# Performance work log

Measured on AMD Instinct MI355X. Metric: run time of the kernel, lower is better.

Reference implementation:

```python
import jax, jax.numpy as jnp
import numpy as np

BETA = 0.25
K = 1024   # num_codebook_vectors
D = 256    # latent_dim


def setup_inputs() -> dict:
    key = jax.random.key(0)
    k1, k2 = jax.random.split(key)
    z = jax.random.normal(k1, (16, D, 64, 64), dtype=jnp.float32)
    # embedding initialized uniform(-1/K, 1/K) as in the torch module
    emb = jax.random.uniform(k2, (K, D), dtype=jnp.float32, minval=-1.0 / K, maxval=1.0 / K)
    return {"z": z, "emb": emb}


def reference(z, emb):
    sg = jax.lax.stop_gradient
    # NCHW -> NHWC
    z_nhwc = jnp.transpose(z, (0, 2, 3, 1))            # [B,H,W,D]
    zf = z_nhwc.reshape(-1, D)                          # [N,D]
    # squared euclidean distances: ||z||^2 + ||e||^2 - 2 z e^T
    d = (jnp.sum(zf * zf, axis=1, keepdims=True)
         + jnp.sum(emb * emb, axis=1)
         - 2.0 * jnp.matmul(zf, emb.T))                 # [N,K]
    min_encoding_indices = jnp.argmin(d, axis=1)        # [N] int
    z_q = emb[min_encoding_indices].reshape(z_nhwc.shape)  # [B,H,W,D]
    # loss exactly as in source (first term is zero in value, faithful)
    loss = (jnp.mean((sg(z_nhwc) - z_nhwc) ** 2)
            + BETA * jnp.mean((z_q - sg(z_nhwc)) ** 2))
    # straight-through estimator
    z_q_st = z_nhwc + sg(z_q - z_nhwc)
    out = jnp.transpose(z_q_st, (0, 3, 1, 2))           # NHWC -> NCHW
    return out, min_encoding_indices, loss
```

## Files before the change

### kernel.cpp

```cpp
#include <hip/hip_runtime.h>

#define DD 256
#define KK 1024
#define HW 4096
#define NROWSZ 65536
#define OUT_Z 16777216
#define OUT_IDX OUT_Z
#define OUT_LOSS (OUT_Z + NROWSZ)

#define MARGIN 4.5e-4f

#define WS_ESQ   0
#define WS_EH    4096
#define WS_HLIST 528384
#define WS_HCNT  790528
#define WS_LSUM  790536
#define WS_EMBT  791552
#define WS_EHP   1840128


typedef _Float16 f16x8 __attribute__((ext_vector_type(8)));
typedef float f32x4 __attribute__((ext_vector_type(4)));
union U16x8 { uint4 u; f16x8 h; };
typedef unsigned long long u64;

static __device__ __forceinline__ u64 umin64(u64 a, u64 b) { return a < b ? a : b; }
static __device__ __forceinline__ unsigned pk16(float a, float b) {
    _Float16 ha = (_Float16)a, hb = (_Float16)b;
    return (unsigned)__builtin_bit_cast(unsigned short, ha)
         | ((unsigned)__builtin_bit_cast(unsigned short, hb) << 16);
}

__global__ void vq_prep(const float* __restrict__ emb, float* __restrict__ esq,
                        uint2* __restrict__ eh2, int* __restrict__ hcnt,
                        double* __restrict__ lsum, float* __restrict__ embT,
                        int use_embT, uint4* __restrict__ ehP, int use_ehp)
{
    const int bid = blockIdx.x;
    const int t = threadIdx.x;
    if (bid == 0 && t == 0) { *hcnt = 0; *lsum = 0.0; }

    if (bid < 4) {
        int k = bid * 256 + t;
        const float* e = emb + (size_t)k * DD;
        float blk[2];
#pragma unroll
        for (int b2 = 0; b2 < 2; ++b2) {
            const float* p = e + b2 * 128;
            float r[8];
#pragma unroll
            for (int j = 0; j < 8; ++j) r[j] = __fmul_rn(p[j], p[j]);
            for (int i = 8; i < 128; i += 8) {
#pragma unroll
                for (int j = 0; j < 8; ++j)
                    r[j] = __fadd_rn(r[j], __fmul_rn(p[i + j], p[i + j]));
            }
            blk[b2] = __fadd_rn(__fadd_rn(__fadd_rn(r[0], r[1]), __fadd_rn(r[2], r[3])),
                                __fadd_rn(__fadd_rn(r[4], r[5]), __fadd_rn(r[6], r[7])));
        }
        esq[k] = __fadd_rn(blk[0], blk[1]);
    } else if (bid < 20) {
        int tid = (bid - 4) * 256 + t;
        const float4* e4 = (const float4*)emb;
#pragma unroll
        for (int i = 0; i < 16; ++i) {
            int idx = i * 4096 + tid;
            float4 v = e4[idx];
            eh2[idx] = make_uint2(pk16(v.x, v.y), pk16(v.z, v.w));
        }
    } else if (bid < 36) {
        if (!use_embT) return;
        int u = bid - 20;
        int k = u * 64 + (t >> 2);
        int c = t & 3;
        const float4* e4 = (const float4*)(emb + (size_t)k * DD);
#pragma unroll
        for (int i = 0; i < 16; ++i) {
            float4 v = e4[c * 16 + i];
            int d = c * 64 + i * 4;
            embT[(size_t)(d + 0) * KK + k] = v.x;
            embT[(size_t)(d + 1) * KK + k] = v.y;
            embT[(size_t)(d + 2) * KK + k] = v.z;
            embT[(size_t)(d + 3) * KK + k] = v.w;
        }
    } else {
        if (!use_ehp) return;
#pragma unroll
        for (int it = 0; it < 8; ++it) {
            int L = ((bid - 36) * 8 + it) * 256 + t;
            int lane = L & 63, ds = (L >> 6) & 7, wcq = (L >> 9) & 1, tt = L >> 10;
            int col = lane & 15, quad = lane >> 4;
            int code = tt * 32 + wcq * 16 + col;
            int d0 = ds * 32 + quad * 8;
            const float* e = emb + (size_t)code * DD + d0;
            float4 a = *(const float4*)e;
            float4 c4 = *(const float4*)(e + 4);
            ehP[L] = make_uint4(pk16(a.x, a.y), pk16(a.z, a.w),
                                pk16(c4.x, c4.y), pk16(c4.z, c4.w));
        }
    }
}

__launch_bounds__(256)
__global__ void vq_zt(const float* __restrict__ z, float* out)
{
    __shared__ __align__(16) char lt[256 * 128];
    uint4* ztF = (uint4*)out;

    const int t = threadIdx.x;
    const int lane = t & 63;
    const int w = t >> 6;
    const int bid = blockIdx.x;
    const int bb = bid >> 6;
    const int hwt = (bid >> 2) & 15;
    const int dt = bid & 3;

    {
        const float* src = z + ((size_t)bb * DD + dt * 64) * HW + hwt * 256 + lane * 4;
#pragma unroll
        for (int i = 0; i < 16; ++i) {
            const int dd = w * 16 + i;
            float4 v = *(const float4*)(src + (size_t)dd * HW);
            float va[4] = {v.x, v.y, v.z, v.w};
#pragma unroll
            for (int c = 0; c < 4; ++c) {
                const int hwl = lane * 4 + c;
                const int sw = ((hwl >> 2) & 7) << 4;
                *(_Float16*)(lt + hwl * 128 + ((dd * 2) ^ sw)) = (_Float16)va[c];
            }
        }
    }
    __syncthreads();

    {
        const size_t gt = (size_t)bb * 64 + hwt * 4 + w;
        const int col = lane & 15, quad = lane >> 4;
#pragma unroll
        for (int f = 0; f < 4; ++f) {
            const int hwl = w * 64 + f * 16 + col;
            const int sw = ((hwl >> 2) & 7) << 4;
#pragma unroll
            for (int dsl = 0; dsl < 2; ++dsl) {
                const int dloc = dsl * 32 + quad * 8;
                uint4 val = *(const uint4*)(lt + hwl * 128 + ((dloc * 2) ^ sw));
                ztF[((gt * 4 + f) * 8 + (dt * 2 + dsl)) * 64 + lane] = val;
            }
        }
    }
}

__launch_bounds__(256, 2)
__global__ void vq_score(float* out, const _Float16* __restrict__ eh,
                         const uint4* __restrict__ ehP, const float* __restrict__ esq,
                         int* __restrict__ hlist, int* __restrict__ hcnt, int use_ehp)
{
    __shared__ float esq_s[1024];
    __shared__ uint2 cand[64][2];

    const uint4* ztF = (const uint4*)out;
    const int t = threadIdx.x;
    const int lane = t & 63;
    const int w = t >> 6;
    const int col = lane & 15;
    const int quad = lane >> 4;
    const int wr = w >> 1;
    const int wc = w & 1;

    const int gt = blockIdx.x;
    const int n0 = gt * 64;

    esq_s[t] = esq[t];
    esq_s[256 + t] = esq[256 + t];
    esq_s[512 + t] = esq[512 + t];
    esq_s[768 + t] = esq[768 + t];

    U16x8 af[2][8];
#pragma unroll
    for (int nt = 0; nt < 2; ++nt) {
        const int f = wr * 2 + nt;
#pragma unroll
        for (int ds = 0; ds < 8; ++ds)
            af[nt][ds].u = ztF[(((size_t)gt * 4 + f) * 8 + ds) * 64 + lane];
    }
    __syncthreads();

    unsigned t1[8], t2[8];
#pragma unroll
    for (int i = 0; i < 8; ++i) { t1[i] = 0xFFFFFFFFu; t2[i] = 0xFFFFFFFFu; }

    if (use_ehp) {
        const uint4* bp = ehP + (size_t)wc * 512 + lane;
#pragma unroll 2
        for (int tt = 0; tt < 32; ++tt) {
            const uint4* p = bp + (size_t)tt * 1024;
            U16x8 bf[8];
#pragma unroll
            for (int ds = 0; ds < 8; ++ds) bf[ds].u = p[ds * 64];
            const int code = tt * 32 + wc * 16 + col;
            const float eq1 = 1.0f + esq_s[code];
            f32x4 acc0 = (f32x4)0.0f, acc1 = (f32x4)0.0f;
#pragma unroll
            for (int ds = 0; ds < 8; ++ds) {
                acc0 = __builtin_amdgcn_mfma_f32_16x16x32_f16(af[0][ds].h, bf[ds].h, acc0, 0, 0, 0);
                acc1 = __builtin_amdgcn_mfma_f32_16x16x32_f16(af[1][ds].h, bf[ds].h, acc1, 0, 0, 0);
            }
#pragma unroll
            for (int r = 0; r < 4; ++r) {
                float s0 = fmaf(-2.0f, acc0[r], eq1);
                unsigned k0 = (__float_as_uint(s0) & 0xFFFFFC00u) | (unsigned)code;
                t2[r] = min(t2[r], max(t1[r], k0));
                t1[r] = min(t1[r], k0);
                float s1 = fmaf(-2.0f, acc1[r], eq1);
                unsigned k1 = (__float_as_uint(s1) & 0xFFFFFC00u) | (unsigned)code;
                t2[4 + r] = min(t2[4 + r], max(t1[4 + r], k1));
                t1[4 + r] = min(t1[4 + r], k1);
            }
        }
    } else {
        const uint4* ehq = (const uint4*)eh;
        for (int tt = 0; tt < 32; ++tt) {
            const int code = tt * 32 + wc * 16 + col;
            const uint4* bp = ehq + (size_t)code * 32 + quad;
            U16x8 bf[8];
#pragma unroll
            for (int ds = 0; ds < 8; ++ds) bf[ds].u = bp[ds * 4];
            const float eq1 = 1.0f + esq_s[code];
            f32x4 acc0 = (f32x4)0.0f, acc1 = (f32x4)0.0f;
#pragma unroll
            for (int ds = 0; ds < 8; ++ds) {
                acc0 = __builtin_amdgcn_mfma_f32_16x16x32_f16(af[0][ds].h, bf[ds].h, acc0, 0, 0, 0);
                acc1 = __builtin_amdgcn_mfma_f32_16x16x32_f16(af[1][ds].h, bf[ds].h, acc1, 0, 0, 0);
            }
#pragma unroll
            for (int r = 0; r < 4; ++r) {
                float s0 = fmaf(-2.0f, acc0[r], eq1);
                unsigned k0 = (__float_as_uint(s0) & 0xFFFFFC00u) | (unsigned)code;
                t2[r] = min(t2[r], max(t1[r], k0));
                t1[r] = min(t1[r], k0);
                float s1 = fmaf(-2.0f, acc1[r], eq1);
                unsigned k1 = (__float_as_uint(s1) & 0xFFFFFC00u) | (unsigned)code;
                t2[4 + r] = min(t2[4 + r], max(t1[4 + r], k1));
                t1[4 + r] = min(t1[4 + r], k1);
            }
        }
    }

#pragma unroll
    for (int mi = 0; mi < 8; ++mi) {
        unsigned a = t1[mi], bb = t2[mi];
#pragma unroll
        for (int off = 1; off < 16; off <<= 1) {
            unsigned o1 = __shfl_xor(a, off, 16);
            unsigned o2 = __shfl_xor(bb, off, 16);
            unsigned mx = max(a, o1);
            a = min(a, o1);
            bb = min(min(bb, o2), mx);
        }
        if (col == 0)
            cand[wr * 32 + (mi >> 2) * 16 + quad * 4 + (mi & 3)][wc] = make_uint2(a, bb);
    }
    __syncthreads();

    if (t < 64) {
        uint2 c0 = cand[t][0], c1 = cand[t][1];
        unsigned mx = max(c0.x, c1.x);
        unsigned a = min(c0.x, c1.x);
        unsigned bb = min(min(c0.y, c1.y), mx);
        float s1 = __uint_as_float(a & 0xFFFFFC00u);
        float s2 = __uint_as_float(bb & 0xFFFFFC00u);
        int k1 = (int)(a & 1023u);
        if (__fsub_rn(s2, s1) > MARGIN) {
            out[OUT_IDX + n0 + t] = (float)k1;
        } else {
            int pos = atomicAdd(hcnt, 1);
            hlist[pos] = n0 + t;
        }
    }
}

template<int USET>
static __device__ __forceinline__ void dot_codes(const float4* __restrict__ embT4,
                                                 const float4* __restrict__ emb4,
                                                 const float4* __restrict__ zb4,
                                                 int t, float (&acc_)[8][4])
{
#pragma unroll 2
    for (int dc = 0; dc < 64; ++dc) {
        float4 e0, e1, e2, e3;
        if (USET) {
            e0 = embT4[(size_t)(dc * 4 + 0) * 256 + t];
            e1 = embT4[(size_t)(dc * 4 + 1) * 256 + t];
            e2 = embT4[(size_t)(dc * 4 + 2) * 256 + t];
            e3 = embT4[(size_t)(dc * 4 + 3) * 256 + t];
        } else {
            float4 a0 = emb4[(size_t)(4 * t + 0) * 64 + dc];
            float4 a1 = emb4[(size_t)(4 * t + 1) * 64 + dc];
            float4 a2 = emb4[(size_t)(4 * t + 2) * 64 + dc];
            float4 a3 = emb4[(size_t)(4 * t + 3) * 64 + dc];
            e0 = make_float4(a0.x, a1.x, a2.x, a3.x);
            e1 = make_float4(a0.y, a1.y, a2.y, a3.y);
            e2 = make_float4(a0.z, a1.z, a2.z, a3.z);
            e3 = make_float4(a0.w, a1.w, a2.w, a3.w);
        }
#pragma unroll
        for (int j = 0; j < 8; ++j) {
            float4 zv = zb4[j * 64 + dc];
            acc_[j][0] = fmaf(zv.x, e0.x, acc_[j][0]);
            acc_[j][1] = fmaf(zv.x, e0.y, acc_[j][1]);
            acc_[j][2] = fmaf(zv.x, e0.z, acc_[j][2]);
            acc_[j][3] = fmaf(zv.x, e0.w, acc_[j][3]);
            acc_[j][0] = fmaf(zv.y, e1.x, acc_[j][0]);
            acc_[j][1] = fmaf(zv.y, e1.y, acc_[j][1]);
            acc_[j][2] = fmaf(zv.y, e1.z, acc_[j][2]);
            acc_[j][3] = fmaf(zv.y, e1.w, acc_[j][3]);
            acc_[j][0] = fmaf(zv.z, e2.x, acc_[j][0]);
            acc_[j][1] = fmaf(zv.z, e2.y, acc_[j][1]);
            acc_[j][2] = fmaf(zv.z, e2.z, acc_[j][2]);
            acc_[j][3] = fmaf(zv.z, e2.w, acc_[j][3]);
            acc_[j][0] = fmaf(zv.w, e3.x, acc_[j][0]);
            acc_[j][1] = fmaf(zv.w, e3.y, acc_[j][1]);
            acc_[j][2] = fmaf(zv.w, e3.z, acc_[j][2]);
            acc_[j][3] = fmaf(zv.w, e3.w, acc_[j][3]);
        }
    }
}

__launch_bounds__(256)
__global__ void vq_hard(const float* __restrict__ z, const float* __restrict__ emb,
                        const float* __restrict__ embT, const float* __restrict__ esq,
                        const int* __restrict__ hlist, const int* __restrict__ hcnt,
                        float* __restrict__ out, int use_embT)
{
    __shared__ __align__(16) float zbuf[8 * 256];
    __shared__ float chains[8][16];
    __shared__ float zq_s[8];
    __shared__ int rows_s[8];
    __shared__ u64 red[4][8];

    const int t = threadIdx.x;
    const int lane = t & 63;
    const int w = t >> 6;
    const int count = *hcnt;

    const float4* embT4 = (const float4*)embT;
    const float4* emb4 = (const float4*)emb;
    const float4* zb4 = (const float4*)zbuf;
    const float4 eqv4 = ((const float4*)esq)[t];
    const float eqa[4] = {eqv4.x, eqv4.y, eqv4.z, eqv4.w};

    for (int g = blockIdx.x; g * 8 < count; g += gridDim.x) {
        __syncthreads();
        if (t < 8) {
            int p = g * 8 + t;
            rows_s[t] = (p < count) ? hlist[p] : -1;
        }
        __syncthreads();

        {
            const int j = t >> 5, dpos = t & 31;
            const int r = rows_s[j];
            float4 v0 = make_float4(0.f, 0.f, 0.f, 0.f), v1 = v0;
            if (r >= 0) {
                const float* zp = z + (size_t)(r >> 12) * (DD * HW) + (r & (HW - 1));
                const int d0 = dpos * 8;
                v0.x = zp[(size_t)(d0 + 0) * HW];
                v0.y = zp[(size_t)(d0 + 1) * HW];
                v0.z = zp[(size_t)(d0 + 2) * HW];
                v0.w = zp[(size_t)(d0 + 3) * HW];
                v1.x = zp[(size_t)(d0 + 4) * HW];
                v1.y = zp[(size_t)(d0 + 5) * HW];
                v1.z = zp[(size_t)(d0 + 6) * HW];
                v1.w = zp[(size_t)(d0 + 7) * HW];
            }
            *(float4*)&zbuf[j * 256 + dpos * 8] = v0;
            *(float4*)&zbuf[j * 256 + dpos * 8 + 4] = v1;
        }
        __syncthreads();

        if (t < 128) {
            int j = t >> 4, c = t & 15, b2 = c >> 3, jj = c & 7;
            const float* p = &zbuf[j * 256];
            int base = b2 * 128 + jj;
            float v = p[base];
            float acc = __fmul_rn(v, v);
            for (int i = 1; i < 16; ++i) {
                float u = p[base + i * 8];
                acc = __fadd_rn(acc, __fmul_rn(u, u));
            }
            chains[j][c] = acc;
        }
        __syncthreads();
        if (t < 8) {
            const float* c = chains[t];
            float b0 = __fadd_rn(__fadd_rn(__fadd_rn(c[0], c[1]), __fadd_rn(c[2], c[3])),
                                 __fadd_rn(__fadd_rn(c[4], c[5]), __fadd_rn(c[6], c[7])));
            float b1 = __fadd_rn(__fadd_rn(__fadd_rn(c[8], c[9]), __fadd_rn(c[10], c[11])),
                                 __fadd_rn(__fadd_rn(c[12], c[13]), __fadd_rn(c[14], c[15])));
            zq_s[t] = __fadd_rn(b0, b1);
        }
        __syncthreads();

        float acc_[8][4];
#pragma unroll
        for (int j = 0; j < 8; ++j)
#pragma unroll
            for (int kk = 0; kk < 4; ++kk) acc_[j][kk] = 0.0f;

        if (use_embT) dot_codes<1>(embT4, emb4, zb4, t, acc_);
        else          dot_codes<0>(embT4, emb4, zb4, t, acc_);

#pragma unroll
        for (int j = 0; j < 8; ++j) {
            u64 m = ~0ull;
#pragma unroll
            for (int kk = 0; kk < 4; ++kk) {
                float s = __fsub_rn(__fadd_rn(zq_s[j], eqa[kk]),
                                    __fmul_rn(2.0f, acc_[j][kk]));
                u64 p = ((u64)__float_as_uint(s) << 32) | (unsigned)(4 * t + kk);
                m = umin64(m, p);
            }
#pragma unroll
            for (int off = 1; off < 64; off <<= 1)
                m = umin64(m, __shfl_xor(m, off, 64));
            if (lane == 0) red[w][j] = m;
        }
        __syncthreads();
        if (t < 8) {
            u64 m = umin64(umin64(red[0][t], red[1][t]), umin64(red[2][t], red[3][t]));
            int r = rows_s[t];
            if (r >= 0) out[OUT_IDX + r] = (float)(int)(m & 0xffffffffu);
        }
    }
}

__launch_bounds__(256)
__global__ void vq_out(const float* __restrict__ z, const float* __restrict__ emb,
                       const float* __restrict__ embT, float* out,
                       double* __restrict__ lsum, int use_embT)
{
    __shared__ float et[8 * 1024];
    __shared__ float wsum[4];

    const int t = threadIdx.x;
    const int lane = t & 63;
    const int w = t >> 6;
    const int bb = blockIdx.x >> 5;
    const int dg = blockIdx.x & 31;

    if (use_embT) {
#pragma unroll
        for (int c = 0; c < 8; ++c)
            *(float4*)&et[c * 1024 + t * 4] =
                *(const float4*)&embT[(size_t)(dg * 8 + c) * KK + t * 4];
    } else {
        for (int i = 0; i < 32; ++i) {
            int kk = i * 256 + t;
            et[kk] = emb[(size_t)(kk & 1023) * DD + dg * 8 + (kk >> 10)];
        }
    }
    __syncthreads();

    float lacc = 0.f;
    const size_t zb = (size_t)bb * DD * HW;
    const float* idxf = out + OUT_IDX + (size_t)bb * HW;
#pragma unroll
    for (int ch = 0; ch < 4; ++ch) {
        const int hw = ch * 1024 + t * 4;
        float4 fi = *(const float4*)&idxf[hw];
        int k0 = (int)fi.x, k1 = (int)fi.y, k2 = (int)fi.z, k3 = (int)fi.w;
#pragma unroll
        for (int dl = 0; dl < 8; ++dl) {
            size_t off = zb + (size_t)(dg * 8 + dl) * HW + hw;
            float4 zv = *(const float4*)&z[off];
            float4 e;
            e.x = et[dl * 1024 + k0];
            e.y = et[dl * 1024 + k1];
            e.z = et[dl * 1024 + k2];
            e.w = et[dl * 1024 + k3];
            *(float4*)&out[off] = e;
            float df;
            df = e.x - zv.x; lacc = fmaf(df, df, lacc);
            df = e.y - zv.y; lacc = fmaf(df, df, lacc);
            df = e.z - zv.z; lacc = fmaf(df, df, lacc);
            df = e.w - zv.w; lacc = fmaf(df, df, lacc);
        }
    }
#pragma unroll
    for (int off = 32; off > 0; off >>= 1) lacc += __shfl_down(lacc, off, 64);
    if (lane == 0) wsum[w] = lacc;
    __syncthreads();
    if (t == 0) {
        double tot = (double)wsum[0] + (double)wsum[1] + (double)wsum[2] + (double)wsum[3];
        atomicAdd(lsum, tot);
    }
}

__global__ void vq_final(const double* __restrict__ lsum, float* __restrict__ out)
{
    out[OUT_LOSS] = (float)(0.25 * (lsum[0] / (double)OUT_Z));
}

extern "C" void kernel_launch(void* const* d_in, const int* in_sizes, int n_in,
                              void* d_out, int out_size, void* d_ws, size_t ws_size,
                              hipStream_t stream)
{
    const float* z = (const float*)d_in[0];
    const float* emb = (const float*)d_in[1];
    float* out = (float*)d_out;
    char* w = (char*)d_ws;

    float* esq = (float*)(w + WS_ESQ);
    _Float16* eh = (_Float16*)(w + WS_EH);
    uint2* eh2 = (uint2*)(w + WS_EH);
    int* hlist = (int*)(w + WS_HLIST);
    int* hcnt = (int*)(w + WS_HCNT);
    double* lsum = (double*)(w + WS_LSUM);
    float* embT = (float*)(w + WS_EMBT);
    uint4* ehP = (uint4*)(w + WS_EHP);

    int use_embT = (ws_size >= (size_t)WS_EMBT + (size_t)DD * KK * sizeof(float)) ? 1 : 0;
    int use_ehp = (ws_size >= (size_t)WS_EHP + (size_t)KK * DD * sizeof(_Float16)) ? 1 : 0;

    vq_prep<<<dim3(52), dim3(256), 0, stream>>>(emb, esq, eh2, hcnt, lsum, embT, use_embT,
                                                ehP, use_ehp);
    vq_zt<<<dim3(1024), dim3(256), 0, stream>>>(z, out);
    vq_score<<<dim3(1024), dim3(256), 0, stream>>>(out, eh, ehP, esq, hlist, hcnt, use_ehp);
    vq_hard<<<dim3(1024), dim3(256), 0, stream>>>(z, emb, embT, esq, hlist, hcnt, out,
                                                  use_embT);
    vq_out<<<dim3(512), dim3(256), 0, stream>>>(z, emb, embT, out, lsum, use_embT);
    vq_final<<<dim3(1), dim3(1), 0, stream>>>(lsum, out);
}
```

Measured before the change: 271.9 us.

## Fuse z transpose into scoring kernel with larger 256-row tiles

Removes the separate vq_zt pass, which wrote an fp16 transposed copy of z into the output buffer for the scoring kernel to read back. vq_score now loads fp32 z directly, converts it to fp16 and stores it transposed in a 128KB swizzled LDS tile. Each 512-thread block now scores 256 rows, four 16-row tiles per wave, so every codebook fragment it loads is reused by more MFMAs. In exchange, the large LDS footprint limits each CU to one block across only 256 blocks. The global-to-LDS load phase is also not overlapped with compute, and accumulator register pressure rises.

```diff
diff --git a/kernel.cpp b/kernel.cpp
--- a/kernel.cpp
+++ b/kernel.cpp
@@ -17,7 +17,6 @@
 #define WS_LSUM  790536
 #define WS_EMBT  791552
 #define WS_EHP   1840128
-
 
 typedef _Float16 f16x8 __attribute__((ext_vector_type(8)));
 typedef float f32x4 __attribute__((ext_vector_type(4)));
@@ -101,63 +100,16 @@
     }
 }
 
-__launch_bounds__(256)
-__global__ void vq_zt(const float* __restrict__ z, float* out)
-{
-    __shared__ __align__(16) char lt[256 * 128];
-    uint4* ztF = (uint4*)out;
-
-    const int t = threadIdx.x;
-    const int lane = t & 63;
-    const int w = t >> 6;
-    const int bid = blockIdx.x;
-    const int bb = bid >> 6;
-    const int hwt = (bid >> 2) & 15;
-    const int dt = bid & 3;
-
-    {
-        const float* src = z + ((size_t)bb * DD + dt * 64) * HW + hwt * 256 + lane * 4;
-#pragma unroll
-        for (int i = 0; i < 16; ++i) {
-            const int dd = w * 16 + i;
-            float4 v = *(const float4*)(src + (size_t)dd * HW);
-            float va[4] = {v.x, v.y, v.z, v.w};
-#pragma unroll
-            for (int c = 0; c < 4; ++c) {
-                const int hwl = lane * 4 + c;
-                const int sw = ((hwl >> 2) & 7) << 4;
-                *(_Float16*)(lt + hwl * 128 + ((dd * 2) ^ sw)) = (_Float16)va[c];
-            }
-        }
-    }
-    __syncthreads();
-
-    {
-        const size_t gt = (size_t)bb * 64 + hwt * 4 + w;
-        const int col = lane & 15, quad = lane >> 4;
-#pragma unroll
-        for (int f = 0; f < 4; ++f) {
-            const int hwl = w * 64 + f * 16 + col;
-            const int sw = ((hwl >> 2) & 7) << 4;
-#pragma unroll
-            for (int dsl = 0; dsl < 2; ++dsl) {
-                const int dloc = dsl * 32 + quad * 8;
-                uint4 val = *(const uint4*)(lt + hwl * 128 + ((dloc * 2) ^ sw));
-                ztF[((gt * 4 + f) * 8 + (dt * 2 + dsl)) * 64 + lane] = val;
-            }
-        }
-    }
-}
-
-__launch_bounds__(256, 2)
-__global__ void vq_score(float* out, const _Float16* __restrict__ eh,
+__launch_bounds__(512, 2)
+__global__ void vq_score(const float* __restrict__ z, const _Float16* __restrict__ eh,
                          const uint4* __restrict__ ehP, const float* __restrict__ esq,
-                         int* __restrict__ hlist, int* __restrict__ hcnt, int use_ehp)
-{
+                         float* __restrict__ out, int* __restrict__ hlist,
+                         int* __restrict__ hcnt, int use_ehp)
+{
+    __shared__ __align__(16) char zh[256 * 512];
     __shared__ float esq_s[1024];
-    __shared__ uint2 cand[64][2];
-
-    const uint4* ztF = (const uint4*)out;
+    __shared__ uint2 cand[256][2];
+
     const int t = threadIdx.x;
     const int lane = t & 63;
     const int w = t >> 6;
@@ -166,27 +118,43 @@
     const int wr = w >> 1;
     const int wc = w & 1;
 
-    const int gt = blockIdx.x;
-    const int n0 = gt * 64;
-
-    esq_s[t] = esq[t];
-    esq_s[256 + t] = esq[256 + t];
-    esq_s[512 + t] = esq[512 + t];
-    esq_s[768 + t] = esq[768 + t];
-
-    U16x8 af[2][8];
-#pragma unroll
-    for (int nt = 0; nt < 2; ++nt) {
-        const int f = wr * 2 + nt;
+    const int n0 = blockIdx.x * 256;
+    const int b = n0 >> 12;
+    const int hw0 = n0 & (HW - 1);
+
+    {
+        const float* zb2 = z + (size_t)b * DD * HW + hw0;
+#pragma unroll 4
+        for (int i = 0; i < 32; ++i) {
+            const int d = w * 32 + i;
+            float4 v = *(const float4*)(zb2 + (size_t)d * HW + lane * 4);
+            float va[4] = {v.x, v.y, v.z, v.w};
+#pragma unroll
+            for (int c = 0; c < 4; ++c) {
+                const int row = lane * 4 + c;
+                *(_Float16*)(zh + (size_t)row * 512 + ((d * 2) ^ ((row & 7) << 4)))
+                    = (_Float16)va[c];
+            }
+        }
+        esq_s[t] = esq[t];
+        esq_s[512 + t] = esq[512 + t];
+    }
+    __syncthreads();
+
+    U16x8 af[4][8];
+#pragma unroll
+    for (int nt = 0; nt < 4; ++nt) {
+        const int row = wr * 64 + nt * 16 + col;
+        const int sw = (row & 7) << 4;
 #pragma unroll
         for (int ds = 0; ds < 8; ++ds)
-            af[nt][ds].u = ztF[(((size_t)gt * 4 + f) * 8 + ds) * 64 + lane];
-    }
-    __syncthreads();
-
-    unsigned t1[8], t2[8];
-#pragma unroll
-    for (int i = 0; i < 8; ++i) { t1[i] = 0xFFFFFFFFu; t2[i] = 0xFFFFFFFFu; }
+            af[nt][ds].u = *(const uint4*)(zh + (size_t)row * 512
+                                           + ((ds * 64 + quad * 16) ^ sw));
+    }
+
+    unsigned t1[16], t2[16];
+#pragma unroll
+    for (int i = 0; i < 16; ++i) { t1[i] = 0xFFFFFFFFu; t2[i] = 0xFFFFFFFFu; }
 
     if (use_ehp) {
         const uint4* bp = ehP + (size_t)wc * 512 + lane;
@@ -198,23 +166,25 @@
             for (int ds = 0; ds < 8; ++ds) bf[ds].u = p[ds * 64];
             const int code = tt * 32 + wc * 16 + col;
             const float eq1 = 1.0f + esq_s[code];
-            f32x4 acc0 = (f32x4)0.0f, acc1 = (f32x4)0.0f;
-#pragma unroll
-            for (int ds = 0; ds < 8; ++ds) {
-                acc0 = __builtin_amdgcn_mfma_f32_16x16x32_f16(af[0][ds].h, bf[ds].h, acc0, 0, 0, 0);
-                acc1 = __builtin_amdgcn_mfma_f32_16x16x32_f16(af[1][ds].h, bf[ds].h, acc1, 0, 0, 0);
-            }
-#pragma unroll
-            for (int r = 0; r < 4; ++r) {
-                float s0 = fmaf(-2.0f, acc0[r], eq1);
-                unsigned k0 = (__float_as_uint(s0) & 0xFFFFFC00u) | (unsigned)code;
-                t2[r] = min(t2[r], max(t1[r], k0));
-                t1[r] = min(t1[r], k0);
-                float s1 = fmaf(-2.0f, acc1[r], eq1);
-                unsigned k1 = (__float_as_uint(s1) & 0xFFFFFC00u) | (unsigned)code;
-                t2[4 + r] = min(t2[4 + r], max(t1[4 + r], k1));
-                t1[4 + r] = min(t1[4 + r], k1);
-            }
+            f32x4 acc[4];
+#pragma unroll
+            for (int nt = 0; nt < 4; ++nt) acc[nt] = (f32x4)0.0f;
+#pragma unroll
+            for (int ds = 0; ds < 8; ++ds)
+#pragma unroll
+                for (int nt = 0; nt < 4; ++nt)
+                    acc[nt] = __builtin_amdgcn_mfma_f32_16x16x32_f16(af[nt][ds].h, bf[ds].h,
+                                                                     acc[nt], 0, 0, 0);
+#pragma unroll
+            for (int nt = 0; nt < 4; ++nt)
+#pragma unroll
+                for (int r = 0; r < 4; ++r) {
+                    float s = fmaf(-2.0f, acc[nt][r], eq1);
+                    unsigned k = (__float_as_uint(s) & 0xFFFFFC00u) | (unsigned)code;
+                    int mi = nt * 4 + r;
+                    t2[mi] = min(t2[mi], max(t1[mi], k));
+                    t1[mi] = min(t1[mi], k);
+                }
         }
     } else {
         const uint4* ehq = (const uint4*)eh;
@@ -225,28 +195,30 @@
 #pragma unroll
             for (int ds = 0; ds < 8; ++ds) bf[ds].u = bp[ds * 4];
             const float eq1 = 1.0f + esq_s[code];
-            f32x4 acc0 = (f32x4)0.0f, acc1 = (f32x4)0.0f;
-#pragma unroll
-            for (int ds = 0; ds < 8; ++ds) {
-                acc0 = __builtin_amdgcn_mfma_f32_16x16x32_f16(af[0][ds].h, bf[ds].h, acc0, 0, 0, 0);
-                acc1 = __builtin_amdgcn_mfma_f32_16x16x32_f16(af[1][ds].h, bf[ds].h, acc1, 0, 0, 0);
-            }
-#pragma unroll
-            for (int r = 0; r < 4; ++r) {
-                float s0 = fmaf(-2.0f, acc0[r], eq1);
-                unsigned k0 = (__float_as_uint(s0) & 0xFFFFFC00u) | (unsigned)code;
-                t2[r] = min(t2[r], max(t1[r], k0));
-                t1[r] = min(t1[r], k0);
-                float s1 = fmaf(-2.0f, acc1[r], eq1);
-                unsigned k1 = (__float_as_uint(s1) & 0xFFFFFC00u) | (unsigned)code;
-                t2[4 + r] = min(t2[4 + r], max(t1[4 + r], k1));
-                t1[4 + r] = min(t1[4 + r], k1);
-            }
-        }
-    }
-
-#pragma unroll
-    for (int mi = 0; mi < 8; ++mi) {
+            f32x4 acc[4];
+#pragma unroll
+            for (int nt = 0; nt < 4; ++nt) acc[nt] = (f32x4)0.0f;
+#pragma unroll
+            for (int ds = 0; ds < 8; ++ds)
+#pragma unroll
+                for (int nt = 0; nt < 4; ++nt)
+                    acc[nt] = __builtin_amdgcn_mfma_f32_16x16x32_f16(af[nt][ds].h, bf[ds].h,
+                                                                     acc[nt], 0, 0, 0);
+#pragma unroll
+            for (int nt = 0; nt < 4; ++nt)
+#pragma unroll
+                for (int r = 0; r < 4; ++r) {
+                    float s = fmaf(-2.0f, acc[nt][r], eq1);
+                    unsigned k = (__float_as_uint(s) & 0xFFFFFC00u) | (unsigned)code;
+                    int mi = nt * 4 + r;
+                    t2[mi] = min(t2[mi], max(t1[mi], k));
+                    t1[mi] = min(t1[mi], k);
+                }
+        }
+    }
+
+#pragma unroll
+    for (int mi = 0; mi < 16; ++mi) {
         unsigned a = t1[mi], bb = t2[mi];
 #pragma unroll
         for (int off = 1; off < 16; off <<= 1) {
@@ -257,11 +229,11 @@
             bb = min(min(bb, o2), mx);
         }
         if (col == 0)
-            cand[wr * 32 + (mi >> 2) * 16 + quad * 4 + (mi & 3)][wc] = make_uint2(a, bb);
+            cand[wr * 64 + (mi >> 2) * 16 + quad * 4 + (mi & 3)][wc] = make_uint2(a, bb);
     }
     __syncthreads();
 
-    if (t < 64) {
+    if (t < 256) {
         uint2 c0 = cand[t][0], c1 = cand[t][1];
         unsigned mx = max(c0.x, c1.x);
         unsigned a = min(c0.x, c1.x);
@@ -523,8 +495,8 @@
 
     vq_prep<<<dim3(52), dim3(256), 0, stream>>>(emb, esq, eh2, hcnt, lsum, embT, use_embT,
                                                 ehP, use_ehp);
-    vq_zt<<<dim3(1024), dim3(256), 0, stream>>>(z, out);
-    vq_score<<<dim3(1024), dim3(256), 0, stream>>>(out, eh, ehP, esq, hlist, hcnt, use_ehp);
+    vq_score<<<dim3(256), dim3(512), 0, stream>>>(z, eh, ehP, esq, out, hlist, hcnt,
+                                                  use_ehp);
     vq_hard<<<dim3(1024), dim3(256), 0, stream>>>(z, emb, embT, esq, hlist, hcnt, out,
                                                   use_embT);
     vq_out<<<dim3(512), dim3(256), 0, stream>>>(z, emb, embT, out, lsum, use_embT);
```

Result: faster. 245.0 us (-9.9%).
